# Kernel tuning notes

Hardware: AMD Instinct MI355X
Metric: run time of the kernel (lower is better)

The kernel has to match this reference:

```python
import jax, jax.numpy as jnp
import numpy as np

B, S, C, L, E, A, H = 4, 4, 4, 512, 64, 32, 8


def _xavier(k, shape, fan_in, fan_out):
    lim = float(np.sqrt(6.0 / (fan_in + fan_out)))
    return jax.random.uniform(k, shape, jnp.float32, -lim, lim)


def setup_inputs() -> dict:
    key = jax.random.key(0)
    ks = jax.random.split(key, 14)
    inp = {
        "query_sequences": jax.random.normal(ks[0], (B, S, L, E), jnp.float32),
        "key_sequences": jax.random.normal(ks[1], (B, S, L, E), jnp.float32),
        "value_sequences": jax.random.normal(ks[2], (B, S, L, E), jnp.float32),
        "query_constants": jax.random.normal(ks[3], (B, C, 1, E), jnp.float32),
        "key_constants": jax.random.normal(ks[4], (B, C, 1, E), jnp.float32),
        "value_constants": jax.random.normal(ks[5], (B, C, 1, E), jnp.float32),
        "qw_seq": _xavier(ks[6], (S, H, E, A), E, A),
        "kw_seq": _xavier(ks[7], (S, H, E, A), E, A),
        "vw_seq": _xavier(ks[8], (S, H, E, A), E, A),
        "qw_con": _xavier(ks[9], (C, H, E, A), E, A),
        "kw_con": _xavier(ks[10], (C, H, E, A), E, A),
        "vw_con": _xavier(ks[11], (C, H, E, A), E, A),
        "head_w_seq": _xavier(ks[12], (S, H * A, E), H * A, E),
        "head_w_con": _xavier(ks[13], (C, H * A, E), H * A, E),
        "mask": 1,
    }
    return inp


def reference(query_sequences, key_sequences, value_sequences,
              query_constants, key_constants, value_constants,
              qw_seq, kw_seq, vw_seq, qw_con, kw_con, vw_con,
              head_w_seq, head_w_con, mask):
    # Per-sequence / per-constant, per-head QKV projections
    q_s = jnp.einsum('bsle,shea->bshla', query_sequences, qw_seq)      # [B,S,H,L,A]
    q_c = jnp.einsum('bcle,chea->bchla', query_constants, qw_con)      # [B,C,H,1,A]
    k_s = jnp.einsum('bsle,shea->bhsla', key_sequences, kw_seq).reshape(B, H, S * L, A)
    k_c = jnp.einsum('bcle,chea->bhcla', key_constants, kw_con).reshape(B, H, C, A)
    v_s = jnp.einsum('bsle,shea->bhsla', value_sequences, vw_seq).reshape(B, H, S * L, A)
    v_c = jnp.einsum('bcle,chea->bhcla', value_constants, vw_con).reshape(B, H, C, A)
    k_all = jnp.concatenate([k_s, k_c], axis=2)                        # [B,H,K,A], K=S*L+C
    v_all = jnp.concatenate([v_s, v_c], axis=2)

    scale = 1.0 / jnp.sqrt(jnp.asarray(A, jnp.float32))
    scores_s = jnp.einsum('bshla,bhka->bshlk', q_s, k_all) * scale     # [B,S,H,L,K]
    if mask:
        # block-causal: within each of the S key blocks mask future timesteps;
        # constant columns (time index -1) are always visible.
        kt = jnp.concatenate([jnp.tile(jnp.arange(L), S), jnp.full((C,), -1)])
        m = kt[None, :] > jnp.arange(L)[:, None]                       # [L,K]
        scores_s = jnp.where(m, -jnp.inf, scores_s)
    p_s = jax.nn.softmax(scores_s, axis=-1)
    out_s = jnp.einsum('bshlk,bhka->bslha', p_s, v_all).reshape(B, S, L, H * A)
    seq_out = jnp.einsum('bslf,sfe->bsle', out_s, head_w_seq)          # [B,S,L,E]

    scores_c = jnp.einsum('bchla,bhka->bchlk', q_c, k_all) * scale     # [B,C,H,1,K]
    p_c = jax.nn.softmax(scores_c, axis=-1)
    out_c = jnp.einsum('bchlk,bhka->bclha', p_c, v_all).reshape(B, C, 1, H * A)
    con_out = jnp.einsum('bclf,cfe->bcle', out_c, head_w_con)          # [B,C,1,E]
    return (seq_out, con_out)
```

## Files before the change

### kernel.cpp

```cpp
#include <hip/hip_runtime.h>
#include <hip/hip_bf16.h>

#define B_ 4
#define S_ 4
#define C_ 4
#define L_ 512
#define E_ 64
#define A_ 32
#define H_ 8
#define HA_ 256
#define KREAL 2052
#define KP 2112
#define NKT 33
#define SCALE 0.17677669529663687f
#define SCALE2 0.25503486321392056f
#define M2FIX 12.0f
#define NEGINF (-__builtin_inff())

using bf16  = __bf16;
using bf16x8 = __attribute__((ext_vector_type(8))) __bf16;
using f32x4  = __attribute__((ext_vector_type(4))) float;

#define OFF_QS    0ull
#define OFF_KALL  4194304ull
#define OFF_VT    8519680ull
#define OFF_OUTS  12845056ull
#define OFF_OUTC  17039360ull
#define OFF_CANON 17055744ull

#define C_QC   1572864
#define C_WQC  1772544
#define C_HWS  1969152
#define C_HWC  2034688

__device__ __forceinline__ bool detect_f32(const unsigned int* __restrict__ x0,
                                           int* sh_cnt)
{
  if (threadIdx.x == 0) *sh_cnt = 0;
  __syncthreads();
  int weird = 0;
  for (int i = threadIdx.x; i < 1024; i += blockDim.x) {
    unsigned h = x0[i] & 0xffffu;
    int e = (int)((h >> 7) & 0xFF);
    if (e == 0xFF || e < 0x60 || e > 0x9F) weird++;
  }
  atomicAdd(sh_cnt, weird);
  __syncthreads();
  int cnt = *sh_cnt;
  return __builtin_amdgcn_readfirstlane(cnt) > 256;
}

__device__ __forceinline__ bf16x8 ld8(const void* p, size_t idx, bool isf32) {
  if (isf32) {
    const float* f = (const float*)p + idx;
    float4 lo = *(const float4*)f;
    float4 hi = *(const float4*)(f + 4);
    bf16x8 v;
    v[0] = (bf16)lo.x; v[1] = (bf16)lo.y; v[2] = (bf16)lo.z; v[3] = (bf16)lo.w;
    v[4] = (bf16)hi.x; v[5] = (bf16)hi.y; v[6] = (bf16)hi.z; v[7] = (bf16)hi.w;
    return v;
  }
  return *(const bf16x8*)((const bf16*)p + idx);
}
__device__ __forceinline__ float ldf(const void* p, size_t idx, bool isf32) {
  return isf32 ? ((const float*)p)[idx] : (float)((const bf16*)p)[idx];
}

struct ConvArgs {
  const void* src[4];
  int n[4];
  int off[4];
  const void* x0;
};

__global__ __launch_bounds__(256) void conv_kernel(ConvArgs args, bf16* __restrict__ dst)
{
  __shared__ int sh_cnt;
  bool isf32 = detect_f32((const unsigned int*)args.x0, &sh_cnt);
  int stride = gridDim.x * blockDim.x;
  int t0 = blockIdx.x * blockDim.x + threadIdx.x;
#pragma unroll 1
  for (int seg = 0; seg < 4; ++seg) {
    int n8 = args.n[seg] >> 3;
    bf16x8* d = (bf16x8*)(dst + args.off[seg]);
    const void* s = args.src[seg];
    for (int i = t0; i < n8; i += stride) d[i] = ld8(s, (size_t)i * 8, isf32);
  }
}

__global__ __launch_bounds__(256) void proj_kernel(
    const void* __restrict__ xq, const void* __restrict__ xk, const void* __restrict__ xv,
    const void* __restrict__ kc_in, const void* __restrict__ vc_in,
    const void* __restrict__ wq, const void* __restrict__ wk, const void* __restrict__ wv,
    const void* __restrict__ wkc, const void* __restrict__ wvc,
    bf16* __restrict__ qs, bf16* __restrict__ kall, bf16* __restrict__ vt)
{
  __shared__ int sh_cnt;
  bool isf32 = detect_f32((const unsigned int*)xq, &sh_cnt);
  int bid = blockIdx.x;
  int tid = threadIdx.x;
  if (bid < 256) {
    int b = bid >> 6, s = (bid >> 4) & 3, h = (bid >> 1) & 7, lc = bid & 1;
    __shared__ bf16 wt[3 * 32 * 72];
    __shared__ bf16 v_lds[32 * 264];
    {
      size_t hb = (size_t)(s * H_ + h) * E_ * A_;
      int e = tid >> 2, ac = tid & 3;
      bf16x8 vq = ld8(wq, hb + e * 32 + ac * 8, isf32);
      bf16x8 vk = ld8(wk, hb + e * 32 + ac * 8, isf32);
      bf16x8 vv = ld8(wv, hb + e * 32 + ac * 8, isf32);
#pragma unroll
      for (int j = 0; j < 8; ++j) {
        int a = ac * 8 + j;
        wt[0 * 2304 + a * 72 + e] = vq[j];
        wt[1 * 2304 + a * 72 + e] = vk[j];
        wt[2 * 2304 + a * 72 + e] = vv[j];
      }
    }
    __syncthreads();
    int lane = tid & 63, wave = tid >> 6;
    int quad = lane >> 4, r = lane & 15;
    bf16x8 bq[2][2], bk[2][2], bv[2][2];
#pragma unroll
    for (int kc = 0; kc < 2; ++kc)
#pragma unroll
      for (int nt = 0; nt < 2; ++nt) {
        int off = (nt * 16 + r) * 72 + kc * 32 + quad * 8;
        bq[kc][nt] = *(const bf16x8*)&wt[off];
        bk[kc][nt] = *(const bf16x8*)&wt[2304 + off];
        bv[kc][nt] = *(const bf16x8*)&wt[4608 + off];
      }
    const size_t xbase = (size_t)(b * S_ + s) * L_ * E_;
    const size_t qsb   = (size_t)((b * S_ + s) * H_ + h) * L_ * A_;
    const size_t kab   = (size_t)(b * H_ + h) * KP * A_;
    const size_t vtb   = (size_t)(b * H_ + h) * A_ * KP;
#pragma unroll 1
    for (int i = 0; i < 4; ++i) {
      int lloc0 = (wave * 4 + i) * 16;
      int row0 = lc * 256 + lloc0;
      size_t rowoff = xbase + (size_t)(row0 + r) * E_ + quad * 8;
      bf16x8 aq0 = ld8(xq, rowoff, isf32);
      bf16x8 aq1 = ld8(xq, rowoff + 32, isf32);
      bf16x8 ak0 = ld8(xk, rowoff, isf32);
      bf16x8 ak1 = ld8(xk, rowoff + 32, isf32);
      bf16x8 av0 = ld8(xv, rowoff, isf32);
      bf16x8 av1 = ld8(xv, rowoff + 32, isf32);
#pragma unroll
      for (int nt = 0; nt < 2; ++nt) {
        f32x4 accq = {0.f,0.f,0.f,0.f}, acck = {0.f,0.f,0.f,0.f}, accv = {0.f,0.f,0.f,0.f};
        accq = __builtin_amdgcn_mfma_f32_16x16x32_bf16(aq0, bq[0][nt], accq, 0,0,0);
        accq = __builtin_amdgcn_mfma_f32_16x16x32_bf16(aq1, bq[1][nt], accq, 0,0,0);
        acck = __builtin_amdgcn_mfma_f32_16x16x32_bf16(ak0, bk[0][nt], acck, 0,0,0);
        acck = __builtin_amdgcn_mfma_f32_16x16x32_bf16(ak1, bk[1][nt], acck, 0,0,0);
        accv = __builtin_amdgcn_mfma_f32_16x16x32_bf16(av0, bv[0][nt], accv, 0,0,0);
        accv = __builtin_amdgcn_mfma_f32_16x16x32_bf16(av1, bv[1][nt], accv, 0,0,0);
#pragma unroll
        for (int reg = 0; reg < 4; ++reg) {
          int l = row0 + quad * 4 + reg;
          int a = nt * 16 + r;
          qs[qsb + (size_t)l * A_ + a]              = (bf16)(accq[reg] * SCALE2);
          kall[kab + (size_t)(s * L_ + l) * A_ + a] = (bf16)acck[reg];
          v_lds[a * 264 + lloc0 + quad * 4 + reg]   = (bf16)accv[reg];
        }
      }
    }
    __syncthreads();
    {
      int a = tid >> 3, c8 = tid & 7;
      size_t rb = vtb + (size_t)a * KP + s * L_ + lc * 256;
#pragma unroll
      for (int j = 0; j < 4; ++j) {
        int chunk = j * 8 + c8;
        *(bf16x8*)&vt[rb + chunk * 8] = *(const bf16x8*)&v_lds[a * 264 + chunk * 8];
      }
    }
  } else {
    int cid = bid - 256;
    int b = cid >> 5, c = (cid >> 3) & 3, h = cid & 7;
    if (tid < 32) {
      int a = tid;
      float kacc = 0.f, vacc = 0.f;
#pragma unroll 8
      for (int e = 0; e < E_; ++e) {
        float xke = ldf(kc_in, (b * C_ + c) * E_ + e, isf32);
        float xve = ldf(vc_in, (b * C_ + c) * E_ + e, isf32);
        float wke = ldf(wkc, ((size_t)(c * H_ + h) * E_ + e) * A_ + a, isf32);
        float wve = ldf(wvc, ((size_t)(c * H_ + h) * E_ + e) * A_ + a, isf32);
        kacc += xke * wke;
        vacc += xve * wve;
      }
      kall[((size_t)(b * H_ + h) * KP + (S_ * L_ + c)) * A_ + a] = (bf16)kacc;
      vt[((size_t)(b * H_ + h) * A_ + a) * KP + (S_ * L_ + c)]   = (bf16)vacc;
    }
    if (c == 0) {
      for (int idx = tid; idx < 60 * 32; idx += 256) {
        int k = KREAL + (idx >> 5), a = idx & 31;
        kall[((size_t)(b * H_ + h) * KP + k) * A_ + a] = (bf16)0.f;
        vt[((size_t)(b * H_ + h) * A_ + a) * KP + k]   = (bf16)0.f;
      }
    }
  }
}

__global__ __launch_bounds__(256) void attn_kernel(
    const bf16* __restrict__ qs, const bf16* __restrict__ kall, const bf16* __restrict__ vt,
    const int* __restrict__ maskp, bf16* __restrict__ outs,
    const bf16* __restrict__ canon, float* __restrict__ outc)
{
  __shared__ __attribute__((aligned(16))) bf16 kt_lds[64 * 40];
  __shared__ __attribute__((aligned(16))) bf16 vt_lds[32 * 72];
  __shared__ __attribute__((aligned(16))) bf16 p_lds[4 * 16 * 72];
  int bid = blockIdx.x, tid = threadIdx.x;
  int lane = tid & 63, wave = tid >> 6, quad = lane >> 4, r = lane & 15;
  if (bid < 1024) {
    int qt = bid & 7, h = (bid >> 3) & 7, s = (bid >> 6) & 3, b = (bid >> 8) & 3;
    bool causal = (*maskp != 0);
    int wrow = qt * 64 + wave * 16;
    int lrow = wrow + r;

    const size_t qsb = (size_t)((b * S_ + s) * H_ + h) * L_ * A_;
    bf16x8 aq = *(const bf16x8*)&qs[qsb + (size_t)(wrow + r) * A_ + quad * 8];

    f32x4 o[2];
    { f32x4 z = {0.f,0.f,0.f,0.f}; o[0] = z; o[1] = z; }
    float l_run = 0.f;

    const size_t kbase = (size_t)(b * H_ + h) * KP * A_;
    const size_t vbase = (size_t)(b * H_ + h) * A_ * KP;
    const int pbase = wave * 16 * 72;
    int krow = tid >> 2, c4 = tid & 3;
    int a8 = tid >> 3, c8 = tid & 7;

    auto compute_tile = [&](int kt) {
      int kmod = (kt & 7) * 64;
      if (causal && kt < 32 && kmod >= wrow + 16) return;
      bool fullv = (kt < 32) && (!causal || kmod + 63 <= wrow);
      f32x4 sf[4];
#pragma unroll
      for (int kg = 0; kg < 4; ++kg) {
        bf16x8 ka = *(const bf16x8*)&kt_lds[(kg * 16 + r) * 40 + quad * 8];
        f32x4 z = {0.f,0.f,0.f,0.f};
        sf[kg] = __builtin_amdgcn_mfma_f32_16x16x32_bf16(ka, aq, z, 0,0,0);
      }
      if (!fullv) {
        int thresh = (kt < 32) ? (lrow - kmod) : 3;
#pragma unroll
        for (int kg = 0; kg < 4; ++kg)
#pragma unroll
          for (int reg = 0; reg < 4; ++reg)
            if (kg * 16 + quad * 4 + reg > thresh) sf[kg][reg] = NEGINF;
      }
      float psum = 0.f;
#pragma unroll
      for (int kg = 0; kg < 4; ++kg) {
        float p0 = exp2f(sf[kg][0] - M2FIX);
        float p1 = exp2f(sf[kg][1] - M2FIX);
        float p2 = exp2f(sf[kg][2] - M2FIX);
        float p3 = exp2f(sf[kg][3] - M2FIX);
        psum += (p0 + p1) + (p2 + p3);
        union { bf16 hh[4]; uint2 u2; } pk;
        pk.hh[0] = (bf16)p0; pk.hh[1] = (bf16)p1; pk.hh[2] = (bf16)p2; pk.hh[3] = (bf16)p3;
        *(uint2*)&p_lds[pbase + r * 72 + kg * 16 + quad * 4] = pk.u2;
      }
      psum += __shfl_xor(psum, 16);
      psum += __shfl_xor(psum, 32);
      l_run += psum;
#pragma unroll
      for (int kc2 = 0; kc2 < 2; ++kc2) {
        bf16x8 ap = *(const bf16x8*)&p_lds[pbase + r * 72 + kc2 * 32 + quad * 8];
#pragma unroll
        for (int nt = 0; nt < 2; ++nt) {
          bf16x8 bv = *(const bf16x8*)&vt_lds[(nt * 16 + r) * 72 + kc2 * 32 + quad * 8];
          o[nt] = __builtin_amdgcn_mfma_f32_16x16x32_bf16(ap, bv, o[nt], 0,0,0);
        }
      }
    };

    int qtc = causal ? qt : 7;
    int nact = 4 * (qtc + 1) + 1;
    int gn = 0, mn = 0;
    int ktA = 0, ktB = 0;
    bf16x8 kA = *(const bf16x8*)&kall[kbase + (size_t)krow * A_ + c4 * 8];
    bf16x8 vA = *(const bf16x8*)&vt[vbase + (size_t)a8 * KP + c8 * 8];
#pragma unroll 1
    for (int i = 0; i < nact; i += 2) {
      bf16x8 kB, vB;
      if (i + 1 < nact) {
        mn++; if (mn > qtc) { mn = 0; gn++; }
        ktB = (gn >= 4) ? 32 : gn * 8 + mn;
        kB = *(const bf16x8*)&kall[kbase + (size_t)(ktB * 64 + krow) * A_ + c4 * 8];
        vB = *(const bf16x8*)&vt[vbase + (size_t)a8 * KP + ktB * 64 + c8 * 8];
      }
      __syncthreads();
      *(bf16x8*)&kt_lds[krow * 40 + c4 * 8] = kA;
      *(bf16x8*)&vt_lds[a8 * 72 + c8 * 8]  = vA;
      __syncthreads();
      compute_tile(ktA);
      if (i + 1 >= nact) break;
      if (i + 2 < nact) {
        mn++; if (mn > qtc) { mn = 0; gn++; }
        ktA = (gn >= 4) ? 32 : gn * 8 + mn;
        kA = *(const bf16x8*)&kall[kbase + (size_t)(ktA * 64 + krow) * A_ + c4 * 8];
        vA = *(const bf16x8*)&vt[vbase + (size_t)a8 * KP + ktA * 64 + c8 * 8];
      }
      __syncthreads();
      *(bf16x8*)&kt_lds[krow * 40 + c4 * 8] = kB;
      *(bf16x8*)&vt_lds[a8 * 72 + c8 * 8]  = vB;
      __syncthreads();
      compute_tile(ktB);
    }
    const size_t obase = (size_t)(b * S_ + s) * L_ * HA_;
#pragma unroll
    for (int reg = 0; reg < 4; ++reg) {
      float lo = __shfl(l_run, (lane & 48) | (quad * 4 + reg));
      int orow = wrow + quad * 4 + reg;
#pragma unroll
      for (int nt = 0; nt < 2; ++nt) {
        int f = h * A_ + nt * 16 + r;
        outs[obase + (size_t)orow * HA_ + f] = (bf16)(o[nt][reg] / lo);
      }
    }
  } else {
    float* parr  = (float*)p_lds;
    float* qsh   = (float*)kt_lds;
    float* red   = (float*)kt_lds + 64;
    float* opart = (float*)kt_lds + 128;
    const bf16* qc  = canon + C_QC;
    const bf16* wqc = canon + C_WQC;
    int cid = bid - 1024;
    int b = cid >> 5, c = (cid >> 3) & 3, h = cid & 7;
    if (tid < 32) {
      float acc = 0.f;
#pragma unroll 8
      for (int e = 0; e < E_; ++e)
        acc += (float)qc[(b * C_ + c) * E_ + e] *
               (float)wqc[((size_t)(c * H_ + h) * E_ + e) * A_ + tid];
      qsh[tid] = acc * SCALE;
    }
    if (tid >= 192 && tid < 192 + (KP - KREAL)) parr[KREAL + tid - 192] = 0.f;
    __syncthreads();
    const size_t kbase = (size_t)(b * H_ + h) * KP * A_;
    float lmax = -1e30f;
#pragma unroll 1
    for (int j = 0; j < 9; ++j) {
      int k = tid + j * 256;
      if (k < KREAL) {
        bf16x8 k0 = *(const bf16x8*)&kall[kbase + (size_t)k * A_ + 0];
        bf16x8 k1 = *(const bf16x8*)&kall[kbase + (size_t)k * A_ + 8];
        bf16x8 k2 = *(const bf16x8*)&kall[kbase + (size_t)k * A_ + 16];
        bf16x8 k3 = *(const bf16x8*)&kall[kbase + (size_t)k * A_ + 24];
        float d = 0.f;
#pragma unroll
        for (int i = 0; i < 8; ++i) {
          d += qsh[i]      * (float)k0[i];
          d += qsh[8 + i]  * (float)k1[i];
          d += qsh[16 + i] * (float)k2[i];
          d += qsh[24 + i] * (float)k3[i];
        }
        parr[k] = d;
        lmax = fmaxf(lmax, d);
      }
    }
#pragma unroll
    for (int dlt = 1; dlt < 64; dlt <<= 1) lmax = fmaxf(lmax, __shfl_xor(lmax, dlt));
    if (lane == 0) red[wave] = lmax;
    __syncthreads();
    float bmax = fmaxf(fmaxf(red[0], red[1]), fmaxf(red[2], red[3]));
    float lsum = 0.f;
#pragma unroll 1
    for (int j = 0; j < 9; ++j) {
      int k = tid + j * 256;
      if (k < KREAL) {
        float p = __expf(parr[k] - bmax);
        parr[k] = p;
        lsum += p;
      }
    }
#pragma unroll
    for (int dlt = 1; dlt < 64; dlt <<= 1) lsum += __shfl_xor(lsum, dlt);
    if (lane == 0) red[4 + wave] = lsum;
    __syncthreads();
    float bsum = (red[4] + red[5]) + (red[6] + red[7]);
    int a = tid >> 3, ch = tid & 7;
    const size_t vbase = (size_t)(b * H_ + h) * A_ * KP + (size_t)a * KP;
    float acc = 0.f;
#pragma unroll 1
    for (int j = 0; j < 33; ++j) {
      int kb = ch * 8 + j * 64;
      bf16x8 vv = *(const bf16x8*)&vt[vbase + kb];
      float4 p0 = *(float4*)&parr[kb];
      float4 p1 = *(float4*)&parr[kb + 4];
      acc += p0.x * (float)vv[0] + p0.y * (float)vv[1] + p0.z * (float)vv[2] + p0.w * (float)vv[3];
      acc += p1.x * (float)vv[4] + p1.y * (float)vv[5] + p1.z * (float)vv[6] + p1.w * (float)vv[7];
    }
    opart[a * 9 + ch] = acc;
    __syncthreads();
    if (tid < 32) {
      float t = 0.f;
#pragma unroll
      for (int i = 0; i < 8; ++i) t += opart[tid * 9 + i];
      outc[(size_t)(b * C_ + c) * HA_ + h * A_ + tid] = t / bsum;
    }
  }
}

__global__ __launch_bounds__(256) void hproj_kernel(
    const bf16* __restrict__ outs, const float* __restrict__ outc,
    const bf16* __restrict__ canon, const unsigned int* __restrict__ x0,
    void* __restrict__ out)
{
  __shared__ __attribute__((aligned(16))) bf16 wt[64 * 264];
  __shared__ int sh_cnt;
  bool isf32 = detect_f32(x0, &sh_cnt);
  int bid = blockIdx.x, tid = threadIdx.x;
  if (bid < 128) {
    const bf16* hw = canon + C_HWS;
    int b = bid >> 5, s = (bid >> 3) & 3, rc = bid & 7;
    for (int idx = tid; idx < HA_ * E_ / 8; idx += 256) {
      int f = idx >> 3, ec = idx & 7;
      bf16x8 v = *(const bf16x8*)&hw[(size_t)s * HA_ * E_ + (size_t)f * E_ + ec * 8];
#pragma unroll
      for (int j = 0; j < 8; ++j) wt[(ec * 8 + j) * 264 + f] = v[j];
    }
    __syncthreads();
    int lane = tid & 63, wave = tid >> 6, quad = lane >> 4, r = lane & 15;
    int row0 = rc * 64 + wave * 16;
    const size_t xbase = (size_t)(b * S_ + s) * L_ * HA_;
    bf16x8 af[8];
#pragma unroll
    for (int kc = 0; kc < 8; ++kc)
      af[kc] = *(const bf16x8*)&outs[xbase + (size_t)(row0 + r) * HA_ + kc * 32 + quad * 8];
#pragma unroll
    for (int nt = 0; nt < 4; ++nt) {
      f32x4 acc = {0.f,0.f,0.f,0.f};
#pragma unroll
      for (int kc = 0; kc < 8; ++kc) {
        bf16x8 bfr = *(const bf16x8*)&wt[(nt * 16 + r) * 264 + kc * 32 + quad * 8];
        acc = __builtin_amdgcn_mfma_f32_16x16x32_bf16(af[kc], bfr, acc, 0,0,0);
      }
#pragma unroll
      for (int reg = 0; reg < 4; ++reg) {
        int row = row0 + quad * 4 + reg;
        int e = nt * 16 + r;
        size_t oidx = ((size_t)(b * S_ + s) * L_ + row) * E_ + e;
        if (isf32) ((float*)out)[oidx] = acc[reg];
        else       ((bf16*)out)[oidx]  = (bf16)acc[reg];
      }
    }
  } else {
    const bf16* hwc = canon + C_HWC;
    float* opart = (float*)wt;
    int i2 = bid - 128;
    int b = i2 >> 2, c = i2 & 3;
    int fc = tid >> 6, e = tid & 63;
    const float* oc = outc + (size_t)(b * C_ + c) * HA_;
    float acc = 0.f;
#pragma unroll 4
    for (int fo = 0; fo < 64; ++fo) {
      int f = fc * 64 + fo;
      acc += oc[f] * (float)hwc[((size_t)c * HA_ + f) * E_ + e];
    }
    opart[fc * 68 + e] = acc;
    __syncthreads();
    if (tid < 64) {
      float t = (opart[0 * 68 + tid] + opart[1 * 68 + tid]) +
                (opart[2 * 68 + tid] + opart[3 * 68 + tid]);
      size_t oidx = (size_t)B_ * S_ * L_ * E_ + (size_t)(b * C_ + c) * E_ + tid;
      if (isf32) ((float*)out)[oidx] = t;
      else       ((bf16*)out)[oidx]  = (bf16)t;
    }
  }
}

extern "C" void kernel_launch(void* const* d_in, const int* in_sizes, int n_in,
                              void* d_out, int out_size, void* d_ws, size_t ws_size,
                              hipStream_t stream) {
  char* ws = (char*)d_ws;
  bf16* qs    = (bf16*)(ws + OFF_QS);
  bf16* kall  = (bf16*)(ws + OFF_KALL);
  bf16* vt    = (bf16*)(ws + OFF_VT);
  bf16* outs  = (bf16*)(ws + OFF_OUTS);
  float* outc = (float*)(ws + OFF_OUTC);
  bf16* canon = (bf16*)(ws + OFF_CANON);
  const int* maskp = (const int*)d_in[14];

  ConvArgs ca;
  const int srcidx[4] = {3, 9, 12, 13};
  const int offs[4]   = {C_QC, C_WQC, C_HWS, C_HWC};
  for (int i = 0; i < 4; ++i) {
    ca.src[i] = d_in[srcidx[i]];
    ca.n[i]   = in_sizes[srcidx[i]];
    ca.off[i] = offs[i];
  }
  ca.x0 = d_in[0];

  conv_kernel<<<64, 256, 0, stream>>>(ca, canon);
  proj_kernel<<<384, 256, 0, stream>>>(d_in[0], d_in[1], d_in[2], d_in[4], d_in[5],
                                       d_in[6], d_in[7], d_in[8], d_in[10], d_in[11],
                                       qs, kall, vt);
  attn_kernel<<<1152, 256, 0, stream>>>(qs, kall, vt, maskp, outs, canon, outc);
  hproj_kernel<<<144, 256, 0, stream>>>(outs, outc, canon, (const unsigned int*)d_in[0], d_out);
}
```

Measured before the change: 179.6 us.

## Remap attention blocks for causal load balance and drop register prefetch pipeline

Block indices are remapped so the head varies fastest and query-tile indices are staggered and mirrored across batches. The intent is to balance the causal workload across concurrently scheduled blocks. The double-buffered register prefetch of K/V tiles is replaced by a simple loop that loads each tile into LDS synchronously and skips tiles beyond the block's causal extent. This simplifies control flow and lowers register pressure, but global load latency is no longer hidden behind compute.

```diff
diff --git a/kernel.cpp b/kernel.cpp
--- a/kernel.cpp
+++ b/kernel.cpp
@@ -213,10 +213,16 @@
   int bid = blockIdx.x, tid = threadIdx.x;
   int lane = tid & 63, wave = tid >> 6, quad = lane >> 4, r = lane & 15;
   if (bid < 1024) {
-    int qt = bid & 7, h = (bid >> 3) & 7, s = (bid >> 6) & 3, b = (bid >> 8) & 3;
+    int h = bid & 7;
+    int q0 = (bid >> 3) & 7;
+    int s = (bid >> 6) & 3;
+    int b = (bid >> 8) & 3;
+    int base = (q0 + 2 * (b >> 1)) & 7;
+    int qt = (b & 1) ? 7 - base : base;
     bool causal = (*maskp != 0);
     int wrow = qt * 64 + wave * 16;
     int lrow = wrow + r;
+    int blockmax = qt * 64 + 63;
 
     const size_t qsb = (size_t)((b * S_ + s) * H_ + h) * L_ * A_;
     bf16x8 aq = *(const bf16x8*)&qs[qsb + (size_t)(wrow + r) * A_ + quad * 8];
@@ -228,13 +234,24 @@
     const size_t kbase = (size_t)(b * H_ + h) * KP * A_;
     const size_t vbase = (size_t)(b * H_ + h) * A_ * KP;
     const int pbase = wave * 16 * 72;
-    int krow = tid >> 2, c4 = tid & 3;
-    int a8 = tid >> 3, c8 = tid & 7;
-
-    auto compute_tile = [&](int kt) {
+
+#pragma unroll 1
+    for (int kt = 0; kt < NKT; ++kt) {
       int kmod = (kt & 7) * 64;
-      if (causal && kt < 32 && kmod >= wrow + 16) return;
+      if (causal && kt < 32 && kmod > blockmax) continue;
+      __syncthreads();
+      {
+        int krow = tid >> 2, c4 = tid & 3;
+        *(bf16x8*)&kt_lds[krow * 40 + c4 * 8] =
+            *(const bf16x8*)&kall[kbase + (size_t)(kt * 64 + krow) * A_ + c4 * 8];
+        int a8 = tid >> 3, c8 = tid & 7;
+        *(bf16x8*)&vt_lds[a8 * 72 + c8 * 8] =
+            *(const bf16x8*)&vt[vbase + (size_t)a8 * KP + kt * 64 + c8 * 8];
+      }
+      __syncthreads();
+      if (causal && kt < 32 && kmod >= wrow + 16) continue;
       bool fullv = (kt < 32) && (!causal || kmod + 63 <= wrow);
+
       f32x4 sf[4];
 #pragma unroll
       for (int kg = 0; kg < 4; ++kg) {
@@ -274,40 +291,6 @@
           o[nt] = __builtin_amdgcn_mfma_f32_16x16x32_bf16(ap, bv, o[nt], 0,0,0);
         }
       }
-    };
-
-    int qtc = causal ? qt : 7;
-    int nact = 4 * (qtc + 1) + 1;
-    int gn = 0, mn = 0;
-    int ktA = 0, ktB = 0;
-    bf16x8 kA = *(const bf16x8*)&kall[kbase + (size_t)krow * A_ + c4 * 8];
-    bf16x8 vA = *(const bf16x8*)&vt[vbase + (size_t)a8 * KP + c8 * 8];
-#pragma unroll 1
-    for (int i = 0; i < nact; i += 2) {
-      bf16x8 kB, vB;
-      if (i + 1 < nact) {
-        mn++; if (mn > qtc) { mn = 0; gn++; }
-        ktB = (gn >= 4) ? 32 : gn * 8 + mn;
-        kB = *(const bf16x8*)&kall[kbase + (size_t)(ktB * 64 + krow) * A_ + c4 * 8];
-        vB = *(const bf16x8*)&vt[vbase + (size_t)a8 * KP + ktB * 64 + c8 * 8];
-      }
-      __syncthreads();
-      *(bf16x8*)&kt_lds[krow * 40 + c4 * 8] = kA;
-      *(bf16x8*)&vt_lds[a8 * 72 + c8 * 8]  = vA;
-      __syncthreads();
-      compute_tile(ktA);
-      if (i + 1 >= nact) break;
-      if (i + 2 < nact) {
-        mn++; if (mn > qtc) { mn = 0; gn++; }
-        ktA = (gn >= 4) ? 32 : gn * 8 + mn;
-        kA = *(const bf16x8*)&kall[kbase + (size_t)(ktA * 64 + krow) * A_ + c4 * 8];
-        vA = *(const bf16x8*)&vt[vbase + (size_t)a8 * KP + ktA * 64 + c8 * 8];
-      }
-      __syncthreads();
-      *(bf16x8*)&kt_lds[krow * 40 + c4 * 8] = kB;
-      *(bf16x8*)&vt_lds[a8 * 72 + c8 * 8]  = vB;
-      __syncthreads();
-      compute_tile(ktB);
     }
     const size_t obase = (size_t)(b * S_ + s) * L_ * HA_;
 #pragma unroll
```

New measurement: 164.1 us. 1.09x faster.
